# Kernel tuning notes

Hardware: AMD Instinct MI355X
Metric: run time of the kernel (lower is better)

## Reference

```python
import jax, jax.numpy as jnp
from jax import lax
import numpy as np

B, N, H = 8, 2048, 128
THRESH = 0.3


def setup_inputs() -> dict:
    key = jax.random.key(0)
    k1, k2, k3 = jax.random.split(key, 3)
    node_embeddings = jax.random.normal(k1, (B * N, H), jnp.float32)
    # contiguous equal-sized graphs, as produced by PyG-style batching
    batch = jnp.repeat(jnp.arange(B, dtype=jnp.int64), N)
    # path_scorer params: Linear(2H->H) then Linear(H->1)
    W1 = jax.random.normal(k2, (2 * H, H), jnp.float32) * 0.02  # input-major
    b1 = jnp.zeros((H,), jnp.float32)
    W2 = jax.random.normal(k3, (H,), jnp.float32) * 0.02
    b2 = jnp.zeros((), jnp.float32)
    return {"node_embeddings": node_embeddings, "batch": batch,
            "W1": W1, "b1": b1, "W2": W2, "b2": b2}


def _run(emb, W1, b1, W2, b2):
    """emb: [B, N, H]. Returns (path [B,N] int32 padded with -1, scores [B,N])."""
    Bn, Nn, Hh = emb.shape
    bidx = jnp.arange(Bn)
    nidx = jnp.arange(Nn)
    # split first Linear: score(i,j) = sigmoid(w2 . elu(e_i@W1a + e_j@W1b + b1) + b2)
    A = jnp.einsum('bnh,hk->bnk', emb, W1[:Hh])          # current-node half [B,N,H]
    C = jnp.einsum('bnh,hk->bnk', emb, W1[Hh:]) + b1     # neighbor half + bias [B,N,H]
    root = jnp.argmax(emb[:, :, 0], axis=1)              # [B]
    visited0 = jnp.zeros((Bn, Nn), bool).at[bidx, root].set(True)

    def step(carry, _):
        cur, visited, active = carry
        # score every node against the current node in one fused pass
        h = jax.nn.elu(A[bidx, cur][:, None, :] + C)                      # [B,N,H]
        s = jax.nn.sigmoid(jnp.einsum('bnh,h->bn', h, W2) + b2)           # [B,N]
        sm = jnp.where(visited, -jnp.inf, s)
        best = jnp.argmax(sm, axis=1)                                     # first max == stable sort
        bscore = jnp.take_along_axis(sm, best[:, None], axis=1)[:, 0]
        take = active & (bscore > THRESH)
        visited = visited | (take[:, None] & (nidx[None, :] == best[:, None]))
        new_cur = jnp.where(take, best, cur)
        step_path = jnp.where(take, best, -1).astype(jnp.int32)
        step_score = jnp.where(take, bscore, 0.0).astype(emb.dtype)
        return (new_cur, visited, take), (step_path, step_score)

    init = (root, visited0, jnp.ones((Bn,), bool))
    _, (paths, scoreseq) = lax.scan(step, init, None, length=Nn - 1)
    path = jnp.concatenate([root[:, None].astype(jnp.int32), paths.T], axis=1)      # [B,N]
    scores = jnp.concatenate([jnp.ones((Bn, 1), emb.dtype), scoreseq.T], axis=1)    # root score = 1.0
    return path, scores


def reference(node_embeddings, batch, W1, b1, W2, b2):
    num_graphs = int(batch[-1]) + 1  # contiguous equal-sized graphs
    emb = node_embeddings.reshape(num_graphs, -1, node_embeddings.shape[-1])
    return _run(emb, W1, b1, W2, b2)
```

## Files before the change

### kernel.cpp

```cpp
#include <hip/hip_runtime.h>
#include <math.h>

#define B_ 8
#define N_ 2048
#define H_ 128
#define BN_ (B_ * N_)


__device__ __forceinline__ float elu1(float x) {
    return x > 0.f ? x : (__expf(x) - 1.f);
}

__device__ __forceinline__ unsigned enc_key(float v) {
    unsigned u = __float_as_uint(v);
    return (u & 0x80000000u) ? ~u : (u | 0x80000000u);
}
__device__ __forceinline__ float dec_key(unsigned k) {
    return __uint_as_float((k & 0x80000000u) ? (k & 0x7FFFFFFFu) : ~k);
}

__global__ __launch_bounds__(H_) void k_ac(const float* __restrict__ emb,
                                           const float* __restrict__ W1,
                                           const float* __restrict__ b1,
                                           float* __restrict__ A,
                                           float* __restrict__ C) {
    __shared__ float e[H_];
    const int i = blockIdx.x;
    const int k = threadIdx.x;
    e[k] = emb[(size_t)i * H_ + k];
    __syncthreads();
    float a = 0.f, c = 0.f;
#pragma unroll 8
    for (int h = 0; h < H_; ++h) {
        const float ev = e[h];
        a = fmaf(ev, W1[h * H_ + k], a);
        c = fmaf(ev, W1[(H_ + h) * H_ + k], c);
    }
    A[(size_t)i * H_ + k] = a;
    C[(size_t)i * H_ + k] = c + b1[k];
}

__global__ __launch_bounds__(256) void k_z(const float* __restrict__ A,
                                           const float* __restrict__ Cc,
                                           const float* __restrict__ w2,
                                           const float* __restrict__ b2p,
                                           unsigned* __restrict__ K) {
    const int lane = threadIdx.x & 63;
    const int wave = threadIdx.x >> 6;
    const int g = blockIdx.x >> 8;
    const int sub = blockIdx.x & 255;
    const int rowtile = sub & 127;
    const int jh = sub >> 7;
    const int ibase = rowtile * 16 + wave * 4;
    const int i = ibase + (lane & 3);
    const int he = (lane >> 2) * 8;
    const float b2v = *b2p;

    const float* Arow = A + ((size_t)g * N_ + i) * H_ + he;
    const float4 a0 = *(const float4*)(Arow);
    const float4 a1 = *(const float4*)(Arow + 4);
    const float4 w0 = *(const float4*)(w2 + he);
    const float4 w1v = *(const float4*)(w2 + he + 4);
    const float* Cg = Cc + (size_t)g * N_ * H_ + he;
    unsigned* Krow = K + ((size_t)g * N_ + i) * N_;
    const bool writer = ((lane >> 2) == 0);

    auto zc = [&](int j) -> float {
        const float* Cj = Cg + (size_t)j * H_;
        const float4 c0 = *(const float4*)(Cj);
        const float4 c1 = *(const float4*)(Cj + 4);
        float p = 0.f;
        p = fmaf(w0.x, elu1(a0.x + c0.x), p);
        p = fmaf(w0.y, elu1(a0.y + c0.y), p);
        p = fmaf(w0.z, elu1(a0.z + c0.z), p);
        p = fmaf(w0.w, elu1(a0.w + c0.w), p);
        p = fmaf(w1v.x, elu1(a1.x + c1.x), p);
        p = fmaf(w1v.y, elu1(a1.y + c1.y), p);
        p = fmaf(w1v.z, elu1(a1.z + c1.z), p);
        p = fmaf(w1v.w, elu1(a1.w + c1.w), p);
        p += __shfl_xor(p, 4);
        p += __shfl_xor(p, 8);
        p += __shfl_xor(p, 16);
        p += __shfl_xor(p, 32);
        return p + b2v;
    };

    const int j0 = jh * 1024;
    for (int j = j0; j < j0 + 1024; j += 4) {
        uint4 kb;
        kb.x = enc_key(zc(j));
        kb.y = enc_key(zc(j + 1));
        kb.z = enc_key(zc(j + 2));
        kb.w = enc_key(zc(j + 3));
        if (writer) *(uint4*)(Krow + j) = kb;
    }
}

__global__ __launch_bounds__(64, 1) void k_path3(const float* __restrict__ emb,
                                                 const unsigned* __restrict__ K,
                                                 float* __restrict__ out) {
    const int g = blockIdx.x;
    const int lane = threadIdx.x;

    unsigned lo[32];
#pragma unroll
    for (int k = 0; k < 8; ++k)
#pragma unroll
        for (int e = 0; e < 4; ++e)
            lo[k * 4 + e] = ~(unsigned)(k * 256 + (lane << 2) + e);

    float bv0 = -INFINITY;
    int bi0 = 0x7fffffff;
    for (int j = lane; j < N_; j += 64) {
        const float v = emb[((size_t)g * N_ + j) * H_];
        if (v > bv0) { bv0 = v; bi0 = j; }
    }
#pragma unroll
    for (int off = 1; off < 64; off <<= 1) {
        const float ov = __shfl_xor(bv0, off);
        const int oi = __shfl_xor(bi0, off);
        if (ov > bv0 || (ov == bv0 && oi < bi0)) { bv0 = ov; bi0 = oi; }
    }
    int cur = bi0;
    unsigned vbits = 0;
    if (((cur >> 2) & 63) == lane)
        vbits |= 1u << (((cur >> 8) << 2) | (cur & 3));

    float* pathOut = out + (size_t)g * N_;
    float* scoreOut = out + (size_t)BN_ + (size_t)g * N_;
    if (lane == 0) {
        pathOut[0] = (float)cur;
        scoreOut[0] = 1.0f;
    }

    const unsigned* Kg = K + (size_t)g * N_ * N_;
    uint4 z[8];
    {
        const uint4* Kr = (const uint4*)(Kg + ((size_t)cur << 11));
#pragma unroll
        for (int k = 0; k < 8; ++k) z[k] = Kr[k * 64 + lane];
    }

    int t = 1;
    for (; t < N_; ++t) {
        unsigned long long kk[32];
#pragma unroll
        for (int k = 0; k < 8; ++k) {
            const unsigned zx = z[k].x, zy = z[k].y, zz = z[k].z, zw = z[k].w;
            const int b = k * 4;
            kk[b + 0] = ((unsigned long long)(((vbits >> (b + 0)) & 1u) ? 0u : zx) << 32) | lo[b + 0];
            kk[b + 1] = ((unsigned long long)(((vbits >> (b + 1)) & 1u) ? 0u : zy) << 32) | lo[b + 1];
            kk[b + 2] = ((unsigned long long)(((vbits >> (b + 2)) & 1u) ? 0u : zz) << 32) | lo[b + 2];
            kk[b + 3] = ((unsigned long long)(((vbits >> (b + 3)) & 1u) ? 0u : zw) << 32) | lo[b + 3];
        }
#pragma unroll
        for (int s = 16; s >= 1; s >>= 1)
#pragma unroll
            for (int i = 0; i < s; ++i)
                if (kk[i + s] > kk[i]) kk[i] = kk[i + s];
        unsigned long long key = kk[0];
#pragma unroll
        for (int off = 1; off < 64; off <<= 1) {
            const unsigned long long ok = __shfl_xor(key, off);
            if (ok > key) key = ok;
        }
        const int bi = (int)(~(unsigned)key);

        {
            const uint4* Kr = (const uint4*)(Kg + ((size_t)bi << 11));
#pragma unroll
            for (int k = 0; k < 8; ++k) z[k] = Kr[k * 64 + lane];
        }

        const float bv = dec_key((unsigned)(key >> 32));
        const float s = 1.f / (1.f + expf(-bv));
        if (!((double)s > 0.3)) break;
        cur = bi;
        if (((cur >> 2) & 63) == lane)
            vbits |= 1u << (((cur >> 8) << 2) | (cur & 3));
        if (lane == 0) {
            pathOut[t] = (float)cur;
            scoreOut[t] = s;
        }
    }
    for (int tt = t + lane; tt < N_; tt += 64) {
        pathOut[tt] = -1.f;
        scoreOut[tt] = 0.f;
    }
}

__device__ __forceinline__ void blockArgmax(float& bv, int& bi, float* rv, int* ri,
                                            int lane, int wid, int nw) {
#pragma unroll
    for (int off = 1; off < 64; off <<= 1) {
        const float ov = __shfl_xor(bv, off);
        const int oi = __shfl_xor(bi, off);
        if (ov > bv || (ov == bv && oi < bi)) { bv = ov; bi = oi; }
    }
    if (lane == 0) { rv[wid] = bv; ri[wid] = bi; }
    __syncthreads();
    if (wid == 0) {
        float v = (lane < nw) ? rv[lane] : -INFINITY;
        int ix = (lane < nw) ? ri[lane] : 0x7fffffff;
#pragma unroll
        for (int off = 1; off < 16; off <<= 1) {
            const float ov = __shfl_xor(v, off);
            const int oi = __shfl_xor(ix, off);
            if (ov > v || (ov == v && oi < ix)) { v = ov; ix = oi; }
        }
        if (lane == 0) { rv[0] = v; ri[0] = ix; }
    }
    __syncthreads();
    bv = rv[0];
    bi = ri[0];
}

__global__ __launch_bounds__(1024) void k_path_fly(const float* __restrict__ emb,
                                                   const float* __restrict__ A,
                                                   const float* __restrict__ Cc,
                                                   const float* __restrict__ w2g,
                                                   const float* __restrict__ b2p,
                                                   float* __restrict__ out) {
    const int g = blockIdx.x;
    const int tid = threadIdx.x;
    const int lane = tid & 63, wid = tid >> 6;
    __shared__ float acur[H_], w2s[H_];
    __shared__ unsigned char vis[N_];
    __shared__ float rv[16];
    __shared__ int ri[16];
    const float b2v = *b2p;
    if (tid < H_) w2s[tid] = w2g[tid];
    for (int j = tid; j < N_; j += 1024) vis[j] = 0;

    float bv = -INFINITY;
    int bi = 0x7fffffff;
    for (int j = tid; j < N_; j += 1024) {
        const float v = emb[((size_t)g * N_ + j) * H_];
        if (v > bv) { bv = v; bi = j; }
    }
    __syncthreads();
    blockArgmax(bv, bi, rv, ri, lane, wid, 16);
    int cur = bi;
    float* pathOut = out + (size_t)g * N_;
    float* scoreOut = out + (size_t)BN_ + (size_t)g * N_;
    if (tid == 0) {
        vis[cur] = 1;
        pathOut[0] = (float)cur;
        scoreOut[0] = 1.0f;
    }
    __syncthreads();

    int t = 1;
    for (; t < N_; ++t) {
        if (tid < H_) acur[tid] = A[((size_t)g * N_ + cur) * H_ + tid];
        __syncthreads();
        float mbv = -INFINITY;
        int mbi = 0x7fffffff;
#pragma unroll
        for (int q = 0; q < 2; ++q) {
            const int j = tid + q * 1024;
            const float* Cj = Cc + ((size_t)g * N_ + j) * H_;
            float p = 0.f;
            for (int h = 0; h < H_; h += 4) {
                const float4 c = *(const float4*)(Cj + h);
                p = fmaf(w2s[h + 0], elu1(acur[h + 0] + c.x), p);
                p = fmaf(w2s[h + 1], elu1(acur[h + 1] + c.y), p);
                p = fmaf(w2s[h + 2], elu1(acur[h + 2] + c.z), p);
                p = fmaf(w2s[h + 3], elu1(acur[h + 3] + c.w), p);
            }
            const float z = p + b2v;
            if (!vis[j] && (z > mbv || (z == mbv && j < mbi))) { mbv = z; mbi = j; }
        }
        __syncthreads();
        blockArgmax(mbv, mbi, rv, ri, lane, wid, 16);
        const float s = 1.f / (1.f + expf(-mbv));
        if (!((double)s > 0.3)) break;
        cur = mbi;
        if (tid == 0) {
            vis[cur] = 1;
            pathOut[t] = (float)cur;
            scoreOut[t] = s;
        }
        __syncthreads();
    }
    for (int tt = t + tid; tt < N_; tt += 1024) {
        pathOut[tt] = -1.f;
        scoreOut[tt] = 0.f;
    }
}

extern "C" void kernel_launch(void* const* d_in, const int* in_sizes, int n_in,
                              void* d_out, int out_size, void* d_ws, size_t ws_size,
                              hipStream_t stream) {
    (void)in_sizes; (void)n_in; (void)out_size;
    const float* emb = (const float*)d_in[0];
    const float* W1 = (const float*)d_in[2];
    const float* b1 = (const float*)d_in[3];
    const float* w2 = (const float*)d_in[4];
    const float* b2 = (const float*)d_in[5];
    float* out = (float*)d_out;

    float* A = (float*)d_ws;
    float* C = A + (size_t)BN_ * H_;
    unsigned* K = (unsigned*)(C + (size_t)BN_ * H_);
    const size_t need = ((size_t)BN_ * H_ * 2 + (size_t)B_ * N_ * N_) * sizeof(float);

    hipLaunchKernelGGL(k_ac, dim3(BN_), dim3(H_), 0, stream, emb, W1, b1, A, C);
    if (ws_size >= need) {
        hipLaunchKernelGGL(k_z, dim3(2048), dim3(256), 0, stream, A, C, w2, b2, K);
        hipLaunchKernelGGL(k_path3, dim3(B_), dim3(64), 0, stream, emb, K, out);
    } else {
        hipLaunchKernelGGL(k_path_fly, dim3(B_), dim3(1024), 0, stream,
                           emb, A, C, w2, b2, out);
    }
}
```

Baseline: 3.257 ms.

## Speculatively prefetch runner-up row in greedy path walk; batch score loads

```diff
diff --git a/kernel.cpp b/kernel.cpp
--- a/kernel.cpp
+++ b/kernel.cpp
@@ -65,38 +65,54 @@
     unsigned* Krow = K + ((size_t)g * N_ + i) * N_;
     const bool writer = ((lane >> 2) == 0);
 
-    auto zc = [&](int j) -> float {
-        const float* Cj = Cg + (size_t)j * H_;
-        const float4 c0 = *(const float4*)(Cj);
-        const float4 c1 = *(const float4*)(Cj + 4);
-        float p = 0.f;
-        p = fmaf(w0.x, elu1(a0.x + c0.x), p);
-        p = fmaf(w0.y, elu1(a0.y + c0.y), p);
-        p = fmaf(w0.z, elu1(a0.z + c0.z), p);
-        p = fmaf(w0.w, elu1(a0.w + c0.w), p);
-        p = fmaf(w1v.x, elu1(a1.x + c1.x), p);
-        p = fmaf(w1v.y, elu1(a1.y + c1.y), p);
-        p = fmaf(w1v.z, elu1(a1.z + c1.z), p);
-        p = fmaf(w1v.w, elu1(a1.w + c1.w), p);
-        p += __shfl_xor(p, 4);
-        p += __shfl_xor(p, 8);
-        p += __shfl_xor(p, 16);
-        p += __shfl_xor(p, 32);
-        return p + b2v;
-    };
-
     const int j0 = jh * 1024;
-    for (int j = j0; j < j0 + 1024; j += 4) {
-        uint4 kb;
-        kb.x = enc_key(zc(j));
-        kb.y = enc_key(zc(j + 1));
-        kb.z = enc_key(zc(j + 2));
-        kb.w = enc_key(zc(j + 3));
-        if (writer) *(uint4*)(Krow + j) = kb;
-    }
-}
-
-__global__ __launch_bounds__(64, 1) void k_path3(const float* __restrict__ emb,
+    for (int j = j0; j < j0 + 1024; j += 8) {
+        float4 c0[8], c1[8];
+#pragma unroll
+        for (int q = 0; q < 8; ++q) {
+            const float* Cj = Cg + (size_t)(j + q) * H_;
+            c0[q] = *(const float4*)(Cj);
+            c1[q] = *(const float4*)(Cj + 4);
+        }
+        float pv[8];
+#pragma unroll
+        for (int q = 0; q < 8; ++q) {
+            float p = 0.f;
+            p = fmaf(w0.x, elu1(a0.x + c0[q].x), p);
+            p = fmaf(w0.y, elu1(a0.y + c0[q].y), p);
+            p = fmaf(w0.z, elu1(a0.z + c0[q].z), p);
+            p = fmaf(w0.w, elu1(a0.w + c0[q].w), p);
+            p = fmaf(w1v.x, elu1(a1.x + c1[q].x), p);
+            p = fmaf(w1v.y, elu1(a1.y + c1[q].y), p);
+            p = fmaf(w1v.z, elu1(a1.z + c1[q].z), p);
+            p = fmaf(w1v.w, elu1(a1.w + c1[q].w), p);
+            pv[q] = p;
+        }
+#pragma unroll
+        for (int q = 0; q < 8; ++q) pv[q] += __shfl_xor(pv[q], 4);
+#pragma unroll
+        for (int q = 0; q < 8; ++q) pv[q] += __shfl_xor(pv[q], 8);
+#pragma unroll
+        for (int q = 0; q < 8; ++q) pv[q] += __shfl_xor(pv[q], 16);
+#pragma unroll
+        for (int q = 0; q < 8; ++q) pv[q] += __shfl_xor(pv[q], 32);
+        if (writer) {
+            uint4 ka, kb;
+            ka.x = enc_key(pv[0] + b2v);
+            ka.y = enc_key(pv[1] + b2v);
+            ka.z = enc_key(pv[2] + b2v);
+            ka.w = enc_key(pv[3] + b2v);
+            kb.x = enc_key(pv[4] + b2v);
+            kb.y = enc_key(pv[5] + b2v);
+            kb.z = enc_key(pv[6] + b2v);
+            kb.w = enc_key(pv[7] + b2v);
+            *(uint4*)(Krow + j) = ka;
+            *(uint4*)(Krow + j + 4) = kb;
+        }
+    }
+}
+
+__global__ __launch_bounds__(64, 1) void k_path4(const float* __restrict__ emb,
                                                  const unsigned* __restrict__ K,
                                                  float* __restrict__ out) {
     const int g = blockIdx.x;
@@ -134,12 +150,13 @@
     }
 
     const unsigned* Kg = K + (size_t)g * N_ * N_;
-    uint4 z[8];
+    uint4 z[8], z2[8];
     {
         const uint4* Kr = (const uint4*)(Kg + ((size_t)cur << 11));
 #pragma unroll
         for (int k = 0; k < 8; ++k) z[k] = Kr[k * 64 + lane];
     }
+    int pred = -1;
 
     int t = 1;
     for (; t < N_; ++t) {
@@ -158,7 +175,8 @@
 #pragma unroll
             for (int i = 0; i < s; ++i)
                 if (kk[i + s] > kk[i]) kk[i] = kk[i + s];
-        unsigned long long key = kk[0];
+        const unsigned long long lanebest = kk[0];
+        unsigned long long key = lanebest;
 #pragma unroll
         for (int off = 1; off < 64; off <<= 1) {
             const unsigned long long ok = __shfl_xor(key, off);
@@ -166,11 +184,29 @@
         }
         const int bi = (int)(~(unsigned)key);
 
+        if (bi == pred) {
+#pragma unroll
+            for (int k = 0; k < 8; ++k) z[k] = z2[k];
+        } else {
+            const uint4* Kr = (const uint4*)(Kg + ((size_t)bi << 11));
+#pragma unroll
+            for (int k = 0; k < 8; ++k) z[k] = Kr[k * 64 + lane];
+        }
+
+        unsigned long long pk = (lanebest == key) ? 0ull : lanebest;
+#pragma unroll
+        for (int off = 1; off < 64; off <<= 1) {
+            const unsigned long long ok = __shfl_xor(pk, off);
+            if (ok > pk) pk = ok;
+        }
+        int np = (pk == 0ull) ? -1 : (int)(~(unsigned)pk);
         {
-            const uint4* Kr = (const uint4*)(Kg + ((size_t)bi << 11));
-#pragma unroll
-            for (int k = 0; k < 8; ++k) z[k] = Kr[k * 64 + lane];
-        }
+            const int safe = (np >= 0) ? np : bi;
+            const uint4* Kr2 = (const uint4*)(Kg + ((size_t)safe << 11));
+#pragma unroll
+            for (int k = 0; k < 8; ++k) z2[k] = Kr2[k * 64 + lane];
+        }
+        pred = np;
 
         const float bv = dec_key((unsigned)(key >> 32));
         const float s = 1.f / (1.f + expf(-bv));
@@ -308,7 +344,7 @@
     hipLaunchKernelGGL(k_ac, dim3(BN_), dim3(H_), 0, stream, emb, W1, b1, A, C);
     if (ws_size >= need) {
         hipLaunchKernelGGL(k_z, dim3(2048), dim3(256), 0, stream, A, C, w2, b2, K);
-        hipLaunchKernelGGL(k_path3, dim3(B_), dim3(64), 0, stream, emb, K, out);
+        hipLaunchKernelGGL(k_path4, dim3(B_), dim3(64), 0, stream, emb, K, out);
     } else {
         hipLaunchKernelGGL(k_path_fly, dim3(B_), dim3(1024), 0, stream,
                            emb, A, C, w2, b2, out);
```

Result: slower. 3.730 ms (+14.5%).
